# Kernel tuning notes

Hardware: AMD Instinct MI355X
Metric: run time of the kernel (lower is better)

Reference implementation:

```python
import jax, jax.numpy as jnp
import numpy as np

CUTOFF = 5.0
NUM_RADIAL = 6
HIDDEN = 128
N_NODES = 100000
N_EDGES = 800000
MAX_Z = 95
P = 6  # envelope_exponent(5) + 1, per PyG Envelope


def _envelope(x):
    # PyG DimeNet Envelope: (1/x + a*x^(p-1) + b*x^p + c*x^(p+1)) * (x < 1)
    a = -(P + 1) * (P + 2) / 2.0   # -28
    b = P * (P + 2)                # 48
    c = -P * (P + 1) / 2.0         # -21
    xp0 = x ** (P - 1)
    xp1 = xp0 * x
    xp2 = xp1 * x
    return (1.0 / x + a * xp0 + b * xp1 + c * xp2) * (x < 1.0)


def setup_inputs():
    key = jax.random.key(0)
    ks = jax.random.split(key, 8)
    z = jax.random.randint(ks[0], (N_NODES,), 0, MAX_Z, dtype=jnp.int32)
    pos = jax.random.normal(ks[1], (N_NODES, 3), dtype=jnp.float32)
    ei = jax.random.randint(ks[2], (2, N_EDGES), 0, N_NODES, dtype=jnp.int32)
    i, j = ei[0], ei[1]
    j = jnp.where(j == i, (j + 1) % N_NODES, j)  # radius_graph emits no self-loops (avoids d=0)
    edge_index = jnp.stack([i, j])
    # BesselBasisLayer learnable frequencies: pi * n
    freq = np.pi * jnp.arange(1, NUM_RADIAL + 1, dtype=jnp.float32)
    s3 = float(np.sqrt(3.0))
    emb_table = jax.random.uniform(ks[3], (MAX_Z, HIDDEN), jnp.float32, -s3, s3)
    W_rbf = jax.random.normal(ks[4], (NUM_RADIAL, HIDDEN), jnp.float32) * (1.0 / np.sqrt(NUM_RADIAL))
    b_rbf = jnp.zeros((HIDDEN,), jnp.float32)
    W_lin = jax.random.normal(ks[5], (3 * HIDDEN, HIDDEN), jnp.float32) * (1.0 / np.sqrt(3 * HIDDEN))
    b_lin = jnp.zeros((HIDDEN,), jnp.float32)
    return {"z": z, "pos": pos, "edge_index": edge_index, "freq": freq,
            "emb_table": emb_table, "W_rbf": W_rbf, "b_rbf": b_rbf,
            "W_lin": W_lin, "b_lin": b_lin}


def reference(z, pos, edge_index, freq, emb_table, W_rbf, b_rbf, W_lin, b_lin):
    n = z.shape[0]
    i, j = edge_index[0], edge_index[1]
    # per-edge distance  [E]
    d = jnp.sqrt(jnp.sum((pos[i] - pos[j]) ** 2, axis=-1))
    # Bessel RBF  [E, num_radial]
    x = d[:, None] / CUTOFF
    rbf = _envelope(x) * jnp.sin(freq * x)
    # DimeNet EmbeddingBlock (act = SiLU/swish)
    h_rbf = jax.nn.silu(rbf @ W_rbf + b_rbf)            # [E, H]
    xz = emb_table[z]                                    # [N, H]
    e_emb = jax.nn.silu(
        jnp.concatenate([xz[i], xz[j], h_rbf], axis=-1) @ W_lin + b_lin
    )                                                    # [E, H]
    # scatter_mean over target node j -> [N, H]
    sums = jax.ops.segment_sum(e_emb, j, num_segments=n)
    cnt = jax.ops.segment_sum(jnp.ones_like(d), j, num_segments=n)
    v_emb = sums / jnp.maximum(cnt, 1.0)[:, None]
    return v_emb  # pool=None -> node-level embeddings
```

## Files before the change

kernel.cpp:

```cpp
#include <hip/hip_runtime.h>
#include <hip/hip_bf16.h>
#include <math.h>

#define HID 128
#define NRAD 6
#define TABN 4096
#define CUTOFF_INV 0.2f
#define MZ 95
#define PAD 32
#define OVF_CAP 65536

typedef unsigned int uint32;

__global__ void build1(const float* __restrict__ emb, const float* __restrict__ W_lin,
                       const float* __restrict__ freq, const float* __restrict__ W_rbf,
                       const float* __restrict__ b_rbf, const float* __restrict__ b_lin,
                       const int* __restrict__ ei, const float* __restrict__ pos,
                       const int* __restrict__ z,
                       __hip_bfloat16* __restrict__ Tb, float* __restrict__ ftab,
                       int* __restrict__ cnt, int* __restrict__ payload,
                       int* __restrict__ ovfcnt, int2* __restrict__ ovfbuf,
                       int MAXZ, int E) {
    __shared__ float sh[HID];
    int h   = threadIdx.x;
    int bid = blockIdx.x;
    int nT  = 2 * MAXZ;
    int nF  = TABN + 1;
    if (bid < nT) {
        int zz = bid >> 1, s = bid & 1;
        sh[h] = emb[zz * HID + h];
        __syncthreads();
        const float* W = W_lin + (size_t)s * HID * HID;
        float acc = (s == 0) ? b_lin[h] : 0.f;
#pragma unroll 8
        for (int k = 0; k < HID; ++k) acc = fmaf(sh[k], W[k * HID + h], acc);
        Tb[(size_t)(s * MAXZ + zz) * HID + h] = __float2bfloat16(acc);
    } else if (bid < nT + nF) {
        int t = bid - nT;
        float rbf[NRAD];
        if (t == 0) {
#pragma unroll
            for (int k = 0; k < NRAD; ++k) rbf[k] = freq[k];
        } else if (t >= TABN) {
#pragma unroll
            for (int k = 0; k < NRAD; ++k) rbf[k] = 0.f;
        } else {
            float x  = (float)t / (float)TABN;
            float x2 = x * x, x5 = x2 * x2 * x;
            float env = 1.f / x + x5 * (-28.f + x * (48.f + x * (-21.f)));
#pragma unroll
            for (int k = 0; k < NRAD; ++k) rbf[k] = env * sinf(freq[k] * x);
        }
        float pre = b_rbf[h];
#pragma unroll
        for (int k = 0; k < NRAD; ++k) pre = fmaf(rbf[k], W_rbf[k * HID + h], pre);
        sh[h] = pre / (1.f + __expf(-pre));
        __syncthreads();
        const float* W3 = W_lin + (size_t)2 * HID * HID;
        float acc = 0.f;
#pragma unroll 8
        for (int k = 0; k < HID; ++k) acc = fmaf(sh[k], W3[k * HID + h], acc);
        ftab[(size_t)t * HID + h] = acc;
    } else {
        int e = (bid - nT - nF) * HID + h;
        if (e < E) {
            int i = ei[e];
            int j = ei[E + e];
            float dx = pos[3 * i]     - pos[3 * j];
            float dy = pos[3 * i + 1] - pos[3 * j + 1];
            float dz = pos[3 * i + 2] - pos[3 * j + 2];
            float d  = sqrtf(dx * dx + dy * dy + dz * dz);
            float u  = fminf(d * CUTOFF_INV, 1.0f) * (float)TABN;
            int   ti = (int)(u + 0.5f);
            if (ti > TABN) ti = TABN;
            int pl = ti | (z[i] << 13) | (z[j] << 20);
            int r  = atomicAdd(&cnt[j], 1);
            if (r < PAD) {
                payload[j * PAD + r] = pl;
            } else {
                int o = atomicAdd(ovfcnt, 1);
                if (o < OVF_CAP) ovfbuf[o] = make_int2(j, pl);
            }
        }
    }
}

__launch_bounds__(1024)
__global__ void gather_k(const int* __restrict__ cnt, const int* __restrict__ payload,
                         const uint32* __restrict__ Tb32, const float* __restrict__ ftab,
                         float* __restrict__ out, int N) {
    __shared__ uint32 sT[2 * MZ * (HID / 2)];
    int tid = threadIdx.x;
    for (int k = tid; k < 2 * MZ * (HID / 2); k += 1024) sT[k] = Tb32[k];
    __syncthreads();

    int lane = tid & 63, wv = tid >> 6;
    int h2   = lane * 2;
    const uint32* sT2 = sT + MZ * (HID / 2);
    const float*  ft  = ftab + h2;
    int nCh = (N + 15) >> 4;

    for (int ch = blockIdx.x; ch < nCh; ch += gridDim.x) {
        int n = (ch << 4) + wv;
        if (n >= N) continue;
        int deg = cnt[n];
        int cb  = deg < PAD ? deg : PAD;
        int plv = payload[n * PAD + (lane & (PAD - 1))];

        float a0 = 0.f, a1 = 0.f;
        for (int k = 0; k < cb; ++k) {
            int pl = __builtin_amdgcn_readlane(plv, k);
            int ti = pl & 0x1FFF;
            int zi = (pl >> 13) & 0x7F;
            int zj = (pl >> 20) & 0x7F;
            float2 f  = *(const float2*)(ft + (size_t)ti * HID);
            uint32 u1 = sT[zi * (HID / 2) + lane];
            uint32 u2 = sT2[zj * (HID / 2) + lane];
            float p0 = __uint_as_float(u1 << 16)         + __uint_as_float(u2 << 16)         + f.x;
            float p1 = __uint_as_float(u1 & 0xFFFF0000u) + __uint_as_float(u2 & 0xFFFF0000u) + f.y;
            a0 = fmaf(p0, __builtin_amdgcn_rcpf(1.f + __expf(-p0)), a0);
            a1 = fmaf(p1, __builtin_amdgcn_rcpf(1.f + __expf(-p1)), a1);
        }
        float s = (deg > 0) ? 1.0f / (float)deg : 0.0f;
        float2 o; o.x = a0 * s; o.y = a1 * s;
        *(float2*)(out + (size_t)n * HID + h2) = o;
    }
}

__global__ void fixup_k(const int* __restrict__ ovfcnt, const int2* __restrict__ ovfbuf,
                        const int* __restrict__ cnt, const uint32* __restrict__ Tb32,
                        const float* __restrict__ ftab, float* __restrict__ out, int MAXZ) {
    int nov = *ovfcnt;
    if (nov > OVF_CAP) nov = OVF_CAP;
    int total = nov * 64;
    int stride = gridDim.x * blockDim.x;
    const uint32* T2b = Tb32 + MAXZ * (HID / 2);
    for (int u = blockIdx.x * blockDim.x + threadIdx.x; u < total; u += stride) {
        int ent = u >> 6, lane = u & 63;
        int2 v = ovfbuf[ent];
        int j  = v.x, pl = v.y;
        int ti = pl & 0x1FFF;
        int zi = (pl >> 13) & 0x7F;
        int zj = (pl >> 20) & 0x7F;
        float2 f  = *(const float2*)(ftab + (size_t)ti * HID + lane * 2);
        uint32 u1 = Tb32[zi * (HID / 2) + lane];
        uint32 u2 = T2b[zj * (HID / 2) + lane];
        float p0 = __uint_as_float(u1 << 16)         + __uint_as_float(u2 << 16)         + f.x;
        float p1 = __uint_as_float(u1 & 0xFFFF0000u) + __uint_as_float(u2 & 0xFFFF0000u) + f.y;
        float s  = 1.0f / (float)max(cnt[j], 1);
        atomicAdd(&out[(size_t)j * HID + lane * 2],     p0 * __builtin_amdgcn_rcpf(1.f + __expf(-p0)) * s);
        atomicAdd(&out[(size_t)j * HID + lane * 2 + 1], p1 * __builtin_amdgcn_rcpf(1.f + __expf(-p1)) * s);
    }
}

extern "C" void kernel_launch(void* const* d_in, const int* in_sizes, int n_in,
                              void* d_out, int out_size, void* d_ws, size_t ws_size,
                              hipStream_t stream) {
    const int*   z     = (const int*)d_in[0];
    const float* pos   = (const float*)d_in[1];
    const int*   ei    = (const int*)d_in[2];
    const float* freq  = (const float*)d_in[3];
    const float* emb   = (const float*)d_in[4];
    const float* W_rbf = (const float*)d_in[5];
    const float* b_rbf = (const float*)d_in[6];
    const float* W_lin = (const float*)d_in[7];
    const float* b_lin = (const float*)d_in[8];

    int N    = in_sizes[0];
    int E    = in_sizes[2] / 2;
    int MAXZ = in_sizes[4] / HID;
    float* out = (float*)d_out;

    int N_pad = ((N + 1024) / 1024) * 1024;

    char* ws = (char*)d_ws;
    size_t off = 0;
    auto alloc = [&](size_t bytes) { char* p = ws + off; off = (off + bytes + 255) & ~(size_t)255; return p; };
    int*   cnt     = (int*)alloc((size_t)N_pad * 4);
    int*   ovfcnt  = (int*)alloc(256);
    __hip_bfloat16* Tb = (__hip_bfloat16*)alloc((size_t)2 * MAXZ * HID * 2);
    float* ftab    = (float*)alloc((size_t)(TABN + 1) * HID * 4);
    int*   payload = (int*)alloc((size_t)N_pad * PAD * 4);
    int2*  ovfbuf  = (int2*)alloc((size_t)OVF_CAP * 8);

    hipMemsetAsync(cnt, 0, (size_t)N_pad * 4 + 256, stream);

    int nBuild = 2 * MAXZ + (TABN + 1) + (E + HID - 1) / HID;
    build1<<<nBuild, HID, 0, stream>>>(emb, W_lin, freq, W_rbf, b_rbf, b_lin,
                                       ei, pos, z, Tb, ftab, cnt, payload,
                                       ovfcnt, ovfbuf, MAXZ, E);
    gather_k<<<512, 1024, 0, stream>>>(cnt, payload, (const uint32*)Tb, ftab, out, N);
    fixup_k<<<128, 256, 0, stream>>>(ovfcnt, ovfbuf, cnt, (const uint32*)Tb, ftab, out, MAXZ);
}
```

Baseline: 190.0 us.

## Pack two nodes per wavefront, batch table rows, fold overflow into gather

The gather kernel now gives each 64-lane wavefront two nodes, with each half-wave handling 4 hidden channels per lane via float4 loads. This halves the per-edge loop iterations per node pair and widens the memory accesses. The Bessel table build computes 8 rows per block so each W_lin load is reused across those rows. The separate overflow fixup kernel is removed: nodes with degree above 32 now linearly scan the overflow buffer inside gather, which drops one launch and its float atomics. The cost is possible half-wave divergence when the two nodes' degrees differ, plus an O(overflow) scan per high-degree node.

```diff
diff --git a/kernel.cpp b/kernel.cpp
--- a/kernel.cpp
+++ b/kernel.cpp
@@ -9,6 +9,7 @@
 #define MZ 95
 #define PAD 32
 #define OVF_CAP 65536
+#define FTR 8
 
 typedef unsigned int uint32;
 
@@ -21,11 +22,11 @@
                        int* __restrict__ cnt, int* __restrict__ payload,
                        int* __restrict__ ovfcnt, int2* __restrict__ ovfbuf,
                        int MAXZ, int E) {
-    __shared__ float sh[HID];
+    __shared__ float sh[FTR * HID];
     int h   = threadIdx.x;
     int bid = blockIdx.x;
     int nT  = 2 * MAXZ;
-    int nF  = TABN + 1;
+    int nF  = (TABN + FTR) / FTR;
     if (bid < nT) {
         int zz = bid >> 1, s = bid & 1;
         sh[h] = emb[zz * HID + h];
@@ -36,31 +37,43 @@
         for (int k = 0; k < HID; ++k) acc = fmaf(sh[k], W[k * HID + h], acc);
         Tb[(size_t)(s * MAXZ + zz) * HID + h] = __float2bfloat16(acc);
     } else if (bid < nT + nF) {
-        int t = bid - nT;
-        float rbf[NRAD];
-        if (t == 0) {
-#pragma unroll
-            for (int k = 0; k < NRAD; ++k) rbf[k] = freq[k];
-        } else if (t >= TABN) {
-#pragma unroll
-            for (int k = 0; k < NRAD; ++k) rbf[k] = 0.f;
-        } else {
-            float x  = (float)t / (float)TABN;
-            float x2 = x * x, x5 = x2 * x2 * x;
-            float env = 1.f / x + x5 * (-28.f + x * (48.f + x * (-21.f)));
-#pragma unroll
-            for (int k = 0; k < NRAD; ++k) rbf[k] = env * sinf(freq[k] * x);
-        }
-        float pre = b_rbf[h];
-#pragma unroll
-        for (int k = 0; k < NRAD; ++k) pre = fmaf(rbf[k], W_rbf[k * HID + h], pre);
-        sh[h] = pre / (1.f + __expf(-pre));
+        int t0 = (bid - nT) * FTR;
+        for (int r = 0; r < FTR; ++r) {
+            int t = t0 + r;
+            float rbf[NRAD];
+            if (t == 0) {
+#pragma unroll
+                for (int k = 0; k < NRAD; ++k) rbf[k] = freq[k];
+            } else if (t >= TABN) {
+#pragma unroll
+                for (int k = 0; k < NRAD; ++k) rbf[k] = 0.f;
+            } else {
+                float x  = (float)t / (float)TABN;
+                float x2 = x * x, x5 = x2 * x2 * x;
+                float env = 1.f / x + x5 * (-28.f + x * (48.f + x * (-21.f)));
+#pragma unroll
+                for (int k = 0; k < NRAD; ++k) rbf[k] = env * sinf(freq[k] * x);
+            }
+            float pre = b_rbf[h];
+#pragma unroll
+            for (int k = 0; k < NRAD; ++k) pre = fmaf(rbf[k], W_rbf[k * HID + h], pre);
+            sh[r * HID + h] = pre / (1.f + __expf(-pre));
+        }
         __syncthreads();
         const float* W3 = W_lin + (size_t)2 * HID * HID;
-        float acc = 0.f;
-#pragma unroll 8
-        for (int k = 0; k < HID; ++k) acc = fmaf(sh[k], W3[k * HID + h], acc);
-        ftab[(size_t)t * HID + h] = acc;
+        float acc[FTR];
+#pragma unroll
+        for (int r = 0; r < FTR; ++r) acc[r] = 0.f;
+#pragma unroll 4
+        for (int k = 0; k < HID; ++k) {
+            float w = W3[k * HID + h];
+#pragma unroll
+            for (int r = 0; r < FTR; ++r) acc[r] = fmaf(sh[r * HID + k], w, acc[r]);
+        }
+        for (int r = 0; r < FTR; ++r) {
+            int t = t0 + r;
+            if (t <= TABN) ftab[(size_t)t * HID + h] = acc[r];
+        }
     } else {
         int e = (bid - nT - nF) * HID + h;
         if (e < E) {
@@ -76,7 +89,7 @@
             int pl = ti | (z[i] << 13) | (z[j] << 20);
             int r  = atomicAdd(&cnt[j], 1);
             if (r < PAD) {
-                payload[j * PAD + r] = pl;
+                payload[(size_t)j * PAD + r] = pl;
             } else {
                 int o = atomicAdd(ovfcnt, 1);
                 if (o < OVF_CAP) ovfbuf[o] = make_int2(j, pl);
@@ -85,9 +98,29 @@
     }
 }
 
+#define EDGE_ACC(pl_) do {                                                                    \
+    int ti_ = (pl_) & 0x1FFF;                                                                 \
+    int zi_ = ((pl_) >> 13) & 0x7F;                                                           \
+    int zj_ = ((pl_) >> 20) & 0x7F;                                                           \
+    float4 f_ = *(const float4*)(ftab + (size_t)ti_ * HID + h4);                              \
+    uint32 a0_ = sT[zi_ * (HID / 2) + l2];                                                    \
+    uint32 a1_ = sT[zi_ * (HID / 2) + l2 + 1];                                                \
+    uint32 b0_ = sT[(MZ + zj_) * (HID / 2) + l2];                                             \
+    uint32 b1_ = sT[(MZ + zj_) * (HID / 2) + l2 + 1];                                         \
+    float p0_ = __uint_as_float(a0_ << 16)         + __uint_as_float(b0_ << 16)         + f_.x; \
+    float p1_ = __uint_as_float(a0_ & 0xFFFF0000u) + __uint_as_float(b0_ & 0xFFFF0000u) + f_.y; \
+    float p2_ = __uint_as_float(a1_ << 16)         + __uint_as_float(b1_ << 16)         + f_.z; \
+    float p3_ = __uint_as_float(a1_ & 0xFFFF0000u) + __uint_as_float(b1_ & 0xFFFF0000u) + f_.w; \
+    ax = fmaf(p0_, __builtin_amdgcn_rcpf(1.f + __expf(-p0_)), ax);                            \
+    ay = fmaf(p1_, __builtin_amdgcn_rcpf(1.f + __expf(-p1_)), ay);                            \
+    az = fmaf(p2_, __builtin_amdgcn_rcpf(1.f + __expf(-p2_)), az);                            \
+    aw = fmaf(p3_, __builtin_amdgcn_rcpf(1.f + __expf(-p3_)), aw);                            \
+} while (0)
+
 __launch_bounds__(1024)
 __global__ void gather_k(const int* __restrict__ cnt, const int* __restrict__ payload,
                          const uint32* __restrict__ Tb32, const float* __restrict__ ftab,
+                         const int* __restrict__ ovfcnt, const int2* __restrict__ ovfbuf,
                          float* __restrict__ out, int N) {
     __shared__ uint32 sT[2 * MZ * (HID / 2)];
     int tid = threadIdx.x;
@@ -95,61 +128,50 @@
     __syncthreads();
 
     int lane = tid & 63, wv = tid >> 6;
-    int h2   = lane * 2;
-    const uint32* sT2 = sT + MZ * (HID / 2);
-    const float*  ft  = ftab + h2;
-    int nCh = (N + 15) >> 4;
+    int hi   = (lane >> 5) & 1;
+    int l32  = lane & 31;
+    int h4   = l32 * 4;
+    int l2   = l32 * 2;
+    int nCh  = (N + 31) >> 5;
+    int nov  = *ovfcnt;
+    if (nov > OVF_CAP) nov = OVF_CAP;
 
     for (int ch = blockIdx.x; ch < nCh; ch += gridDim.x) {
-        int n = (ch << 4) + wv;
-        if (n >= N) continue;
-        int deg = cnt[n];
+        int nA = (ch << 5) + (wv << 1);
+        if (nA >= N) continue;
+        int  n      = nA + hi;
+        bool nvalid = (n < N);
+        int deg = 0, plv = 0;
+        if (nvalid) {
+            deg = cnt[n];
+            plv = payload[(size_t)n * PAD + l32];
+        }
         int cb  = deg < PAD ? deg : PAD;
-        int plv = payload[n * PAD + (lane & (PAD - 1))];
-
-        float a0 = 0.f, a1 = 0.f;
-        for (int k = 0; k < cb; ++k) {
-            int pl = __builtin_amdgcn_readlane(plv, k);
-            int ti = pl & 0x1FFF;
-            int zi = (pl >> 13) & 0x7F;
-            int zj = (pl >> 20) & 0x7F;
-            float2 f  = *(const float2*)(ft + (size_t)ti * HID);
-            uint32 u1 = sT[zi * (HID / 2) + lane];
-            uint32 u2 = sT2[zj * (HID / 2) + lane];
-            float p0 = __uint_as_float(u1 << 16)         + __uint_as_float(u2 << 16)         + f.x;
-            float p1 = __uint_as_float(u1 & 0xFFFF0000u) + __uint_as_float(u2 & 0xFFFF0000u) + f.y;
-            a0 = fmaf(p0, __builtin_amdgcn_rcpf(1.f + __expf(-p0)), a0);
-            a1 = fmaf(p1, __builtin_amdgcn_rcpf(1.f + __expf(-p1)), a1);
-        }
-        float s = (deg > 0) ? 1.0f / (float)deg : 0.0f;
-        float2 o; o.x = a0 * s; o.y = a1 * s;
-        *(float2*)(out + (size_t)n * HID + h2) = o;
-    }
-}
-
-__global__ void fixup_k(const int* __restrict__ ovfcnt, const int2* __restrict__ ovfbuf,
-                        const int* __restrict__ cnt, const uint32* __restrict__ Tb32,
-                        const float* __restrict__ ftab, float* __restrict__ out, int MAXZ) {
-    int nov = *ovfcnt;
-    if (nov > OVF_CAP) nov = OVF_CAP;
-    int total = nov * 64;
-    int stride = gridDim.x * blockDim.x;
-    const uint32* T2b = Tb32 + MAXZ * (HID / 2);
-    for (int u = blockIdx.x * blockDim.x + threadIdx.x; u < total; u += stride) {
-        int ent = u >> 6, lane = u & 63;
-        int2 v = ovfbuf[ent];
-        int j  = v.x, pl = v.y;
-        int ti = pl & 0x1FFF;
-        int zi = (pl >> 13) & 0x7F;
-        int zj = (pl >> 20) & 0x7F;
-        float2 f  = *(const float2*)(ftab + (size_t)ti * HID + lane * 2);
-        uint32 u1 = Tb32[zi * (HID / 2) + lane];
-        uint32 u2 = T2b[zj * (HID / 2) + lane];
-        float p0 = __uint_as_float(u1 << 16)         + __uint_as_float(u2 << 16)         + f.x;
-        float p1 = __uint_as_float(u1 & 0xFFFF0000u) + __uint_as_float(u2 & 0xFFFF0000u) + f.y;
-        float s  = 1.0f / (float)max(cnt[j], 1);
-        atomicAdd(&out[(size_t)j * HID + lane * 2],     p0 * __builtin_amdgcn_rcpf(1.f + __expf(-p0)) * s);
-        atomicAdd(&out[(size_t)j * HID + lane * 2 + 1], p1 * __builtin_amdgcn_rcpf(1.f + __expf(-p1)) * s);
+        int cbA = __builtin_amdgcn_readlane(cb, 0);
+        int cbB = __builtin_amdgcn_readlane(cb, 32);
+        int cbm = cbA > cbB ? cbA : cbB;
+
+        float ax = 0.f, ay = 0.f, az = 0.f, aw = 0.f;
+        for (int k = 0; k < cbm; ++k) {
+            int plA = __builtin_amdgcn_readlane(plv, k);
+            int plB = __builtin_amdgcn_readlane(plv, k + 32);
+            int pl  = hi ? plB : plA;
+            if (k < cb) {
+                EDGE_ACC(pl);
+            }
+        }
+        if (deg > PAD && nov > 0) {
+            for (int o = 0; o < nov; ++o) {
+                int2 v = ovfbuf[o];
+                if (v.x == n) { int pl = v.y; EDGE_ACC(pl); }
+            }
+        }
+        if (nvalid) {
+            float s = (deg > 0) ? 1.0f / (float)deg : 0.0f;
+            float4 o4;
+            o4.x = ax * s; o4.y = ay * s; o4.z = az * s; o4.w = aw * s;
+            *(float4*)(out + (size_t)n * HID + h4) = o4;
+        }
     }
 }
 
@@ -185,10 +207,10 @@
 
     hipMemsetAsync(cnt, 0, (size_t)N_pad * 4 + 256, stream);
 
-    int nBuild = 2 * MAXZ + (TABN + 1) + (E + HID - 1) / HID;
+    int nBuild = 2 * MAXZ + (TABN + FTR) / FTR + (E + HID - 1) / HID;
     build1<<<nBuild, HID, 0, stream>>>(emb, W_lin, freq, W_rbf, b_rbf, b_lin,
                                        ei, pos, z, Tb, ftab, cnt, payload,
                                        ovfcnt, ovfbuf, MAXZ, E);
-    gather_k<<<512, 1024, 0, stream>>>(cnt, payload, (const uint32*)Tb, ftab, out, N);
-    fixup_k<<<128, 256, 0, stream>>>(ovfcnt, ovfbuf, cnt, (const uint32*)Tb, ftab, out, MAXZ);
+    gather_k<<<512, 1024, 0, stream>>>(cnt, payload, (const uint32*)Tb, ftab,
+                                       ovfcnt, ovfbuf, out, N);
 }
```

Measured after the change: 190.3 us. No clear change (+0.1%).
